# Optimization experiments

Measured on AMD Instinct MI355X. Metric: run time of the kernel, lower is better.

The kernel has to match this reference:

```python
import jax, jax.numpy as jnp
from jax import lax
import numpy as np

B, A, D = 4, 512, 729   # batch, num_angles, detector pixels
H, W = 512, 512         # reconstruction volume


def setup_inputs() -> dict:
    key = jax.random.key(0)
    sino = jax.random.normal(key, (B, A, D), dtype=jnp.float32)
    vol_spacing = np.array([1.0, 1.0], dtype=np.float32)          # (sy, sx)
    det_spacing = np.array([1.0], dtype=np.float32)
    vol_origin = np.array([-(H - 1) / 2.0, -(W - 1) / 2.0], dtype=np.float32)
    det_origin = np.array([-(D - 1) / 2.0], dtype=np.float32)
    angles = jnp.linspace(0.0, jnp.pi, A, endpoint=False, dtype=jnp.float32)
    return {
        "input": sino,
        "volume_shape": np.array([H, W], dtype=np.int64),
        "volume_origin": jnp.asarray(vol_origin),
        "detector_origin": jnp.asarray(det_origin),
        "volume_spacing": jnpp if False else jnp.asarray(vol_spacing),
        "detector_spacing": jnp.asarray(det_spacing),
        "trajectory": angles,
    }


def _backproject(sino, vol_shape, vol_origin, det_origin, vol_spacing, det_spacing, angles):
    h, w = int(vol_shape[0]), int(vol_shape[1])
    d = sino.shape[-1]
    ys = vol_origin[0] + jnp.arange(h, dtype=sino.dtype) * vol_spacing[0]  # [H]
    xs = vol_origin[1] + jnp.arange(w, dtype=sino.dtype) * vol_spacing[1]  # [W]

    def step(acc, per_angle):
        theta, sino_a = per_angle                      # scalar, [B, D]
        # ray coordinate s = x*cos(theta) + y*sin(theta) for every voxel
        s = xs[None, :] * jnp.cos(theta) + ys[:, None] * jnp.sin(theta)  # [H, W]
        u = (s - det_origin[0]) / det_spacing[0]       # continuous detector index
        u0 = jnp.floor(u)
        frac = u - u0
        i0 = u0.astype(jnp.int32)
        i1 = i0 + 1
        valid0 = (i0 >= 0) & (i0 < d)
        valid1 = (i1 >= 0) & (i1 < d)
        i0c = jnp.clip(i0, 0, d - 1)
        i1c = jnp.clip(i1, 0, d - 1)
        v0 = sino_a[:, i0c]                            # [B, H, W] gather
        v1 = sino_a[:, i1c]                            # [B, H, W] gather
        contrib = (jnp.where(valid0, (1.0 - frac) * v0, 0.0)
                   + jnp.where(valid1, frac * v1, 0.0))
        return acc + contrib, None

    acc0 = jnp.zeros((sino.shape[0], h, w), dtype=sino.dtype)
    out, _ = lax.scan(step, acc0, (angles, jnp.swapaxes(sino, 0, 1)))
    return out


def reference(input, volume_shape, volume_origin, detector_origin,
              volume_spacing, detector_spacing, trajectory):
    return _backproject(input, volume_shape, volume_origin, detector_origin,
                        volume_spacing, detector_spacing, trajectory)
```

## Files before the change

### kernel.cpp

```cpp
#include <hip/hip_runtime.h>
#include <hip/hip_fp16.h>

#define BB 4
#define AA 512
#define ZS 8
#define AH (AA / ZS)
#define DD 729
#define HH 512
#define WW 512
#define CH 4
#define NC (AH / CH)
#define WIN 32

typedef float        f4v  __attribute__((ext_vector_type(4)));
typedef unsigned int u4v8 __attribute__((ext_vector_type(4), aligned(8)));

__device__ inline float buf_load1(__amdgpu_buffer_rsrc_t r, int elem) {
    union { unsigned int u; float f; } c;
    c.u = __builtin_amdgcn_raw_buffer_load_b32(r, elem * 4, 0, 0);
    return c.f;
}
__device__ inline __half2 h2bc(unsigned int x) {
    return __builtin_bit_cast(__half2, x);
}
__device__ inline unsigned int pk2u(float a, float b) {
    return __builtin_bit_cast(unsigned int, __builtin_amdgcn_cvt_pkrtz(a, b));
}

__global__ __launch_bounds__(128, 8) void bp_kernel(
    const float* __restrict__ sino,
    const float* __restrict__ vol_origin,
    const float* __restrict__ det_origin,
    const float* __restrict__ vol_spacing,
    const float* __restrict__ det_spacing,
    const float* __restrict__ angles,
    float* __restrict__ out)
{
    __shared__ f4v          s_csk[2][AH];
    __shared__ int          s_s0[2][AH];
    __shared__ unsigned int s_win[2][CH * WIN * 2];

    const int tid  = threadIdx.y * 16 + threadIdx.x;
    const int lane = tid & 63;
    const int wv   = tid >> 6;

    const float inv_ds = 1.0f / det_spacing[0];
    const int abase = blockIdx.z * AH;

    const int x0 = blockIdx.x * 32 + wv * 16;
    const int y0 = blockIdx.y * 16;
    const float vsx = vol_spacing[1], vsy = vol_spacing[0];
    const float off = -det_origin[0] * inv_ds;
    const float xc = vol_origin[1] + ((float)x0 + 7.5f) * vsx;
    const float yc = vol_origin[0] + ((float)y0 + 7.5f) * vsy;

    {
        const int a = lane;
        float th = angles[abase + a];
        float c = cosf(th) * inv_ds;
        float s = sinf(th) * inv_ds;
        float uc = fmaf(xc, c, fmaf(yc, s, off));
        int s0 = min(max((int)uc - (WIN / 2), 0), DD - WIN);
        f4v k;
        k.x = c; k.y = s; k.z = off - (float)s0; k.w = 4.0f * vsy * s;
        s_csk[wv][a] = k;
        s_s0[wv][a]  = s0;
    }
    __threadfence_block();

    const int ix  = x0 + threadIdx.x;
    const int iy0 = y0 + (threadIdx.y & 3);
    const float xw = vol_origin[1] + (float)ix * vsx;
    const float yw = vol_origin[0] + (float)iy0 * vsy;

    const int hh = lane & 1;
    const int ee = lane >> 1;
    const int gA = (2 * hh) * (AA * DD) + ee;

    const __amdgpu_buffer_rsrc_t rsrc = __builtin_amdgcn_make_buffer_rsrc(
        (void*)sino, (short)0, BB * AA * DD * 4, 0x00020000);

    f4v acc0 = {0.f, 0.f, 0.f, 0.f};
    f4v acc1 = {0.f, 0.f, 0.f, 0.f};
    f4v acc2 = {0.f, 0.f, 0.f, 0.f};
    f4v acc3 = {0.f, 0.f, 0.f, 0.f};

    const __half2 hz   = h2bc(0u);
    const __half2 one2 = h2bc(0x3C003C00u);
    __half2 h01_0 = hz, h23_0 = hz, h01_1 = hz, h23_1 = hz;
    __half2 h01_2 = hz, h23_2 = hz, h01_3 = hz, h23_3 = hz;

    float vA0, vB0, vA1, vB1, vA2, vB2, vA3, vB3;

    #define STAGE_LOAD(C)                                                  \
        do {                                                               \
            const int aa = (C) * CH;                                       \
            const int r0 = (abase + aa + 0) * DD + s_s0[wv][aa + 0] + gA;  \
            const int r1 = (abase + aa + 1) * DD + s_s0[wv][aa + 1] + gA;  \
            const int r2 = (abase + aa + 2) * DD + s_s0[wv][aa + 2] + gA;  \
            const int r3 = (abase + aa + 3) * DD + s_s0[wv][aa + 3] + gA;  \
            vA0 = buf_load1(rsrc, r0); vB0 = buf_load1(rsrc, r0 + AA * DD);\
            vA1 = buf_load1(rsrc, r1); vB1 = buf_load1(rsrc, r1 + AA * DD);\
            vA2 = buf_load1(rsrc, r2); vB2 = buf_load1(rsrc, r2 + AA * DD);\
            vA3 = buf_load1(rsrc, r3); vB3 = buf_load1(rsrc, r3 + AA * DD);\
        } while (0)

    #define CONVERT_WRITE()                                                \
        do {                                                               \
            s_win[wv][0 * 64 + lane] = pk2u(vA0, vB0);                     \
            s_win[wv][1 * 64 + lane] = pk2u(vA1, vB1);                     \
            s_win[wv][2 * 64 + lane] = pk2u(vA2, vB2);                     \
            s_win[wv][3 * 64 + lane] = pk2u(vA3, vB3);                     \
        } while (0)

    #define LERP(U, H01, H23)                                              \
        do {                                                               \
            const int   li = (int)(U);                                     \
            const float fr = __builtin_amdgcn_fractf(U);                   \
            const __half2 fr2 = h2bc(pk2u(fr, fr));                        \
            const __half2 om2 = __hsub2(one2, fr2);                        \
            const u4v8 t = *(const u4v8*)&s_win[wv][(j * WIN + li) * 2];   \
            H01 = __hfma2(h2bc(t.x), om2, __hfma2(h2bc(t.z), fr2, H01));   \
            H23 = __hfma2(h2bc(t.y), om2, __hfma2(h2bc(t.w), fr2, H23));   \
        } while (0)

    #define WIDEN(H01, H23, ACC)                                           \
        do {                                                               \
            (ACC).x += __low2float(H01);  (ACC).y += __high2float(H01);    \
            (ACC).z += __low2float(H23);  (ACC).w += __high2float(H23);    \
            H01 = hz; H23 = hz;                                            \
        } while (0)

    STAGE_LOAD(0);
    for (int c = 0; c < NC; ++c) {
        __threadfence_block();
        CONVERT_WRITE();
        __threadfence_block();
        if (c + 1 < NC) STAGE_LOAD(c + 1);
        #pragma unroll
        for (int j = 0; j < CH; ++j) {
            const f4v  k  = s_csk[wv][c * CH + j];
            const float u0 = fmaf(xw, k.x, fmaf(yw, k.y, k.z));
            const float u1 = u0 + k.w;
            const float u2 = u1 + k.w;
            const float u3 = u2 + k.w;
            LERP(u0, h01_0, h23_0);
            LERP(u1, h01_1, h23_1);
            LERP(u2, h01_2, h23_2);
            LERP(u3, h01_3, h23_3);
        }
        WIDEN(h01_0, h23_0, acc0);
        WIDEN(h01_1, h23_1, acc1);
        WIDEN(h01_2, h23_2, acc2);
        WIDEN(h01_3, h23_3, acc3);
    }
    #undef STAGE_LOAD
    #undef CONVERT_WRITE
    #undef LERP
    #undef WIDEN

    const size_t HW = (size_t)HH * WW;
    #define OUT4(ACC, ROWOFF)                                              \
        do {                                                               \
            const size_t o = (size_t)(iy0 + (ROWOFF)) * WW + ix;           \
            unsafeAtomicAdd(&out[o],          (ACC).x);                    \
            unsafeAtomicAdd(&out[o + HW],     (ACC).y);                    \
            unsafeAtomicAdd(&out[o + 2 * HW], (ACC).z);                    \
            unsafeAtomicAdd(&out[o + 3 * HW], (ACC).w);                    \
        } while (0)
    OUT4(acc0, 0);
    OUT4(acc1, 4);
    OUT4(acc2, 8);
    OUT4(acc3, 12);
    #undef OUT4
}

extern "C" void kernel_launch(void* const* d_in, const int* in_sizes, int n_in,
                              void* d_out, int out_size, void* d_ws, size_t ws_size,
                              hipStream_t stream) {
    const float* sino        = (const float*)d_in[0];
    const float* vol_origin  = (const float*)d_in[2];
    const float* det_origin  = (const float*)d_in[3];
    const float* vol_spacing = (const float*)d_in[4];
    const float* det_spacing = (const float*)d_in[5];
    const float* angles      = (const float*)d_in[6];
    float* out = (float*)d_out;

    hipMemsetAsync(d_out, 0, (size_t)out_size * sizeof(float), stream);

    dim3 block(16, 8, 1);
    dim3 grid(WW / 32, HH / 16, ZS);
    bp_kernel<<<grid, block, 0, stream>>>(sino, vol_origin, det_origin,
                                          vol_spacing, det_spacing, angles, out);
}
```

Measured before the change: 121.8 us.

## Keep per-angle constants in registers via readlane and restage sinogram window loads

```diff
diff --git a/kernel.cpp b/kernel.cpp
--- a/kernel.cpp
+++ b/kernel.cpp
@@ -11,13 +11,15 @@
 #define CH 4
 #define NC (AH / CH)
 #define WIN 32
-
-typedef float        f4v  __attribute__((ext_vector_type(4)));
-typedef unsigned int u4v8 __attribute__((ext_vector_type(4), aligned(8)));
-
-__device__ inline float buf_load1(__amdgpu_buffer_rsrc_t r, int elem) {
+#define AD (AA * DD)
+
+typedef float        f4v   __attribute__((ext_vector_type(4)));
+typedef unsigned int u4v8  __attribute__((ext_vector_type(4), aligned(8)));
+typedef unsigned int u4v16 __attribute__((ext_vector_type(4), aligned(16)));
+
+__device__ inline float buf_load1(__amdgpu_buffer_rsrc_t r, int voff_bytes, int soff) {
     union { unsigned int u; float f; } c;
-    c.u = __builtin_amdgcn_raw_buffer_load_b32(r, elem * 4, 0, 0);
+    c.u = __builtin_amdgcn_raw_buffer_load_b32(r, voff_bytes, soff, 0);
     return c.f;
 }
 __device__ inline __half2 h2bc(unsigned int x) {
@@ -25,6 +27,10 @@
 }
 __device__ inline unsigned int pk2u(float a, float b) {
     return __builtin_bit_cast(unsigned int, __builtin_amdgcn_cvt_pkrtz(a, b));
+}
+__device__ inline float rdlanef(float v, int idx) {
+    return __builtin_bit_cast(float,
+        __builtin_amdgcn_readlane(__builtin_bit_cast(int, v), idx));
 }
 
 __global__ __launch_bounds__(128, 8) void bp_kernel(
@@ -36,8 +42,6 @@
     const float* __restrict__ angles,
     float* __restrict__ out)
 {
-    __shared__ f4v          s_csk[2][AH];
-    __shared__ int          s_s0[2][AH];
     __shared__ unsigned int s_win[2][CH * WIN * 2];
 
     const int tid  = threadIdx.y * 16 + threadIdx.x;
@@ -54,6 +58,8 @@
     const float xc = vol_origin[1] + ((float)x0 + 7.5f) * vsx;
     const float yc = vol_origin[0] + ((float)y0 + 7.5f) * vsy;
 
+    float vkx, vky, vkz, vkw;
+    int   vs0;
     {
         const int a = lane;
         float th = angles[abase + a];
@@ -61,21 +67,21 @@
         float s = sinf(th) * inv_ds;
         float uc = fmaf(xc, c, fmaf(yc, s, off));
         int s0 = min(max((int)uc - (WIN / 2), 0), DD - WIN);
-        f4v k;
-        k.x = c; k.y = s; k.z = off - (float)s0; k.w = 4.0f * vsy * s;
-        s_csk[wv][a] = k;
-        s_s0[wv][a]  = s0;
+        vkx = c;
+        vky = s;
+        vkz = off - (float)s0;
+        vkw = 4.0f * vsy * s;
+        vs0 = s0;
     }
-    __threadfence_block();
 
     const int ix  = x0 + threadIdx.x;
     const int iy0 = y0 + (threadIdx.y & 3);
     const float xw = vol_origin[1] + (float)ix * vsx;
     const float yw = vol_origin[0] + (float)iy0 * vsy;
 
-    const int hh = lane & 1;
-    const int ee = lane >> 1;
-    const int gA = (2 * hh) * (AA * DD) + ee;
+    const int wsel = lane >> 4;
+    const int msel = lane & 15;
+    const int lane_base = wsel * DD + 2 * msel;
 
     const __amdgpu_buffer_rsrc_t rsrc = __builtin_amdgcn_make_buffer_rsrc(
         (void*)sino, (short)0, BB * AA * DD * 4, 0x00020000);
@@ -90,27 +96,36 @@
     __half2 h01_0 = hz, h23_0 = hz, h01_1 = hz, h23_1 = hz;
     __half2 h01_2 = hz, h23_2 = hz, h01_3 = hz, h23_3 = hz;
 
-    float vA0, vB0, vA1, vB1, vA2, vB2, vA3, vB3;
+    float b0x, b0y, b1x, b1y, b2x, b2y, b3x, b3y;
 
     #define STAGE_LOAD(C)                                                  \
         do {                                                               \
             const int aa = (C) * CH;                                       \
-            const int r0 = (abase + aa + 0) * DD + s_s0[wv][aa + 0] + gA;  \
-            const int r1 = (abase + aa + 1) * DD + s_s0[wv][aa + 1] + gA;  \
-            const int r2 = (abase + aa + 2) * DD + s_s0[wv][aa + 2] + gA;  \
-            const int r3 = (abase + aa + 3) * DD + s_s0[wv][aa + 3] + gA;  \
-            vA0 = buf_load1(rsrc, r0); vB0 = buf_load1(rsrc, r0 + AA * DD);\
-            vA1 = buf_load1(rsrc, r1); vB1 = buf_load1(rsrc, r1 + AA * DD);\
-            vA2 = buf_load1(rsrc, r2); vB2 = buf_load1(rsrc, r2 + AA * DD);\
-            vA3 = buf_load1(rsrc, r3); vB3 = buf_load1(rsrc, r3 + AA * DD);\
+            const int t0 = __builtin_amdgcn_readlane(vs0, aa + 0);         \
+            const int t1 = __builtin_amdgcn_readlane(vs0, aa + 1);         \
+            const int t2 = __builtin_amdgcn_readlane(vs0, aa + 2);         \
+            const int t3 = __builtin_amdgcn_readlane(vs0, aa + 3);         \
+            const int s0sel = (lane & 32) ? ((lane & 16) ? t3 : t2)        \
+                                          : ((lane & 16) ? t1 : t0);       \
+            const int va = ((abase + aa) * DD + lane_base + s0sel) * 4;    \
+            b0x = buf_load1(rsrc, va,     0);                              \
+            b0y = buf_load1(rsrc, va + 4, 0);                              \
+            b1x = buf_load1(rsrc, va,     AD * 4);                         \
+            b1y = buf_load1(rsrc, va + 4, AD * 4);                         \
+            b2x = buf_load1(rsrc, va,     2 * AD * 4);                     \
+            b2y = buf_load1(rsrc, va + 4, 2 * AD * 4);                     \
+            b3x = buf_load1(rsrc, va,     3 * AD * 4);                     \
+            b3y = buf_load1(rsrc, va + 4, 3 * AD * 4);                     \
         } while (0)
 
     #define CONVERT_WRITE()                                                \
         do {                                                               \
-            s_win[wv][0 * 64 + lane] = pk2u(vA0, vB0);                     \
-            s_win[wv][1 * 64 + lane] = pk2u(vA1, vB1);                     \
-            s_win[wv][2 * 64 + lane] = pk2u(vA2, vB2);                     \
-            s_win[wv][3 * 64 + lane] = pk2u(vA3, vB3);                     \
+            u4v16 q;                                                       \
+            q.x = pk2u(b0x, b1x);                    \
+            q.y = pk2u(b2x, b3x);                    \
+            q.z = pk2u(b0y, b1y);                    \
+            q.w = pk2u(b2y, b3y);                    \
+            *(u4v16*)&s_win[wv][wsel * 64 + msel * 4] = q;                 \
         } while (0)
 
     #define LERP(U, H01, H23)                                              \
@@ -139,11 +154,15 @@
         if (c + 1 < NC) STAGE_LOAD(c + 1);
         #pragma unroll
         for (int j = 0; j < CH; ++j) {
-            const f4v  k  = s_csk[wv][c * CH + j];
-            const float u0 = fmaf(xw, k.x, fmaf(yw, k.y, k.z));
-            const float u1 = u0 + k.w;
-            const float u2 = u1 + k.w;
-            const float u3 = u2 + k.w;
+            const int ai = c * CH + j;
+            const float kx = rdlanef(vkx, ai);
+            const float ky = rdlanef(vky, ai);
+            const float kz = rdlanef(vkz, ai);
+            const float kw = rdlanef(vkw, ai);
+            const float u0 = fmaf(xw, kx, fmaf(yw, ky, kz));
+            const float u1 = u0 + kw;
+            const float u2 = u1 + kw;
+            const float u3 = u2 + kw;
             LERP(u0, h01_0, h23_0);
             LERP(u1, h01_1, h23_1);
             LERP(u2, h01_2, h23_2);
```

Result: slower. 130.9 us (+7.5%).
